# Optimization experiments

Measured on AMD Instinct MI355X. Metric: run time of the kernel, lower is better.

The kernel has to match this reference:

```python
import jax, jax.numpy as jnp
import numpy as np

H, DH = 16, 64            # num heads, head dim
D = H * DH                # hidden size 1024
ALPHA, BW, A, R = 1.0, 1.0, 0.5, 1.0
D_INT = DH                # num_heads > 1 -> d_intrinsic = head_dim
EPS = 1e-12
CLIP = 1.0 - 1e-6         # keep acos (and its grad) finite


def setup_inputs() -> dict:
    key = jax.random.key(0)
    ks = jax.random.split(key, 5)
    w = lambda k: jax.random.normal(k, (D, D), jnp.float32) * 0.02
    return {
        "x": jax.random.normal(ks[0], (4, 1024, D), jnp.float32),
        "wq": w(ks[1]), "bq": jnp.zeros((D,), jnp.float32),
        "wk": w(ks[2]), "bk": jnp.zeros((D,), jnp.float32),
        "wv": w(ks[3]), "bv": jnp.zeros((D,), jnp.float32),
        "wo": w(ks[4]), "bo": jnp.zeros((D,), jnp.float32),
    }


def reference(x, wq, bq, wk, bk, wv, bv, wo, bo):
    B, S, _ = x.shape

    def heads(t):  # [B,S,D] -> [B,H,S,DH]
        return t.reshape(B, S, H, DH).transpose(0, 2, 1, 3)

    def l2norm(t):
        return t / jnp.maximum(jnp.linalg.norm(t, axis=-1, keepdims=True), EPS)

    q = l2norm(heads(x @ wq + bq))
    k = l2norm(heads(x @ wk + bk))
    v = heads(x @ wv + bv)

    # spherical geodesic distance
    dot = jnp.clip(jnp.einsum('bhqd,bhkd->bhqk', q, k), -CLIP, CLIP)
    g_dist = jnp.arccos(dot) * R

    # power-law kernel (alpha < 2 branch)
    attn_score = (1.0 + g_dist / jnp.sqrt(BW)) ** (-(D_INT + ALPHA))

    # bistochastic (Sinkhorn-like) normalization, a > 0 branch
    n_r = attn_score.sum(-1)   # [B,H,S] row sums
    n_c = attn_score.sum(-2)   # [B,H,S] col sums
    k_tilde = (n_r ** (-A))[..., :, None] * attn_score * (n_c ** (-A))[..., None, :]
    probs = k_tilde / jnp.maximum(k_tilde.sum(-1, keepdims=True), EPS)  # L1 row normalize

    out = jnp.einsum('bhqk,bhkd->bhqd', probs, v)
    out = out.transpose(0, 2, 1, 3).reshape(B, S, D)
    return out @ wo + bo
```

## Files before the change

kernel.cpp:

```cpp
#include <hip/hip_runtime.h>
#include <hip/hip_bf16.h>
#include <cstdint>
#include <cstddef>

#define BATCH  4
#define SEQ    1024
#define NHEAD  16
#define DHEAD  64
#define DMODEL 1024
#define NROWS  4096
#define BH     64
#define CLIPV  0.999999f
#define PEXP   65.0f

#define QOFF   133.5f
#define QK_    490.8988764f
#define QINV   0.0020370716f
#define QC     65535.5f

typedef _Float16 h16;
typedef _Float16 half8 __attribute__((ext_vector_type(8)));
typedef _Float16 half4 __attribute__((ext_vector_type(4)));
typedef __fp16   fp16x2 __attribute__((ext_vector_type(2)));
typedef float    f32x4 __attribute__((ext_vector_type(4)));

typedef const __attribute__((address_space(1))) void gas_void;
typedef __attribute__((address_space(3))) void las_void;
#define GLOAD_LDS16(g, l) \
    __builtin_amdgcn_global_load_lds((gas_void*)(g), (las_void*)(l), 16, 0, 0)

__device__ __forceinline__ float spfns_lg(float d) {
    d = __builtin_amdgcn_fmed3f(d, -CLIPV, CLIPV);
    float a = fabsf(d);
    float s = __builtin_amdgcn_sqrtf(1.0f - a);
    float p = -0.0187293f;
    p = fmaf(p, a,  0.0742610f);
    p = fmaf(p, a, -0.2121144f);
    p = fmaf(p, a,  1.5707288f);
    float r = s * p;
    float g = (d >= 0.0f) ? r : (3.14159265358979f - r);
    return __builtin_amdgcn_logf(1.0f + g);
}

__device__ __forceinline__ unsigned pk_h2(float lo, float hi) {
    fp16x2 v = __builtin_amdgcn_cvt_pkrtz(lo, hi);
    return __builtin_bit_cast(unsigned, v);
}

__global__ __launch_bounds__(256) void cvt_x(const float* __restrict__ x,
                                             h16* __restrict__ xh)
{
    size_t i = ((size_t)blockIdx.x * 256 + threadIdx.x) * 8;
    float4 a = *reinterpret_cast<const float4*>(&x[i]);
    float4 b = *reinterpret_cast<const float4*>(&x[i + 4]);
    half8 o;
    o[0]=(h16)a.x; o[1]=(h16)a.y; o[2]=(h16)a.z; o[3]=(h16)a.w;
    o[4]=(h16)b.x; o[5]=(h16)b.y; o[6]=(h16)b.z; o[7]=(h16)b.w;
    *reinterpret_cast<half8*>(&xh[i]) = o;
}

__global__ __launch_bounds__(256) void wtrans(const float* __restrict__ wq,
                                              const float* __restrict__ wk,
                                              const float* __restrict__ wv,
                                              const float* __restrict__ wo,
                                              h16* __restrict__ wt3,
                                              h16* __restrict__ wot)
{
    __shared__ float T[64][65];
    const int k0 = blockIdx.x * 64, d0 = blockIdx.y * 64, z = blockIdx.z;
    const float* src = (z==0)?wq:(z==1)?wk:(z==2)?wv:wo;
    h16* dst = (z==3) ? wot : (wt3 + (size_t)z * 1024 * 1024);
    const int t = threadIdx.x;

    #pragma unroll
    for (int p = 0; p < 4; ++p) {
        int k = (t >> 4) + p * 16;
        int c = (t & 15) * 4;
        float4 v = *reinterpret_cast<const float4*>(&src[(size_t)(k0 + k) * 1024 + d0 + c]);
        T[c + 0][k] = v.x; T[c + 1][k] = v.y; T[c + 2][k] = v.z; T[c + 3][k] = v.w;
    }
    __syncthreads();
    #pragma unroll
    for (int p = 0; p < 2; ++p) {
        int dl = (t >> 3) + p * 32;
        int c  = (t & 7) * 8;
        half8 o;
        #pragma unroll
        for (int e = 0; e < 8; ++e) o[e] = (h16)T[dl][c + e];
        *reinterpret_cast<half8*>(&dst[(size_t)(d0 + dl) * 1024 + k0 + c]) = o;
    }
}

__global__ __launch_bounds__(256) void gemm_f16(const h16* __restrict__ A,
                                                const h16* __restrict__ Bt,
                                                const float* __restrict__ b0,
                                                const float* __restrict__ b1,
                                                const float* __restrict__ b2,
                                                h16* __restrict__ oq,
                                                h16* __restrict__ ok,
                                                h16* __restrict__ ovt,
                                                float* __restrict__ of32,
                                                int mode)
{
    __shared__ __align__(16) h16 As[128][64];
    __shared__ __align__(16) h16 Bs[128][64];
    const int n0 = blockIdx.x * 128, d0 = blockIdx.y * 128;
    const int t = threadIdx.x, l = t & 63, w = t >> 6;
    const int wr = (w >> 1) * 64, wc = (w & 1) * 64;
    const int lr = l >> 3, lc8 = (l & 7) * 8;

    f32x4 acc[4][4];
    #pragma unroll
    for (int i = 0; i < 4; ++i)
        #pragma unroll
        for (int j = 0; j < 4; ++j) acc[i][j] = (f32x4){0.f,0.f,0.f,0.f};

    for (int k0 = 0; k0 < 1024; k0 += 64) {
        __syncthreads();
        #pragma unroll
        for (int q = 0; q < 4; ++q) {
            int r = w * 32 + q * 8;
            GLOAD_LDS16(&A[(size_t)(n0 + r + lr) * 1024 + k0 + lc8], &As[r][0]);
            GLOAD_LDS16(&Bt[(size_t)(d0 + r + lr) * 1024 + k0 + lc8], &Bs[r][0]);
        }
        __syncthreads();
        #pragma unroll
        for (int kk = 0; kk < 2; ++kk) {
            half8 a[4], b[4];
            #pragma unroll
            for (int fi = 0; fi < 4; ++fi)
                a[fi] = *reinterpret_cast<const half8*>(&As[wr + fi*16 + (l & 15)][((l >> 4) * 8) + kk * 32]);
            #pragma unroll
            for (int fj = 0; fj < 4; ++fj)
                b[fj] = *reinterpret_cast<const half8*>(&Bs[wc + fj*16 + (l & 15)][((l >> 4) * 8) + kk * 32]);
            #pragma unroll
            for (int fi = 0; fi < 4; ++fi)
                #pragma unroll
                for (int fj = 0; fj < 4; ++fj)
                    acc[fi][fj] = __builtin_amdgcn_mfma_f32_16x16x32_f16(a[fi], b[fj], acc[fi][fj], 0, 0, 0);
        }
    }

    if (mode == 0) {
        const int dbase = d0 + wc;
        const int mat = dbase >> 10, d1b = dbase & 1023, h = d1b >> 6;
        const float* bp = (mat == 0) ? b0 : (mat == 1) ? b1 : b2;
        #pragma unroll
        for (int fi = 0; fi < 4; ++fi) {
            float vals[4][4];
            #pragma unroll
            for (int fj = 0; fj < 4; ++fj) {
                float bias = bp[d1b + fj * 16 + (l & 15)];
                #pragma unroll
                for (int rr = 0; rr < 4; ++rr) vals[fj][rr] = acc[fi][fj][rr] + bias;
            }
            if (mat < 2) {
                float ss[4];
                #pragma unroll
                for (int rr = 0; rr < 4; ++rr)
                    ss[rr] = vals[0][rr]*vals[0][rr] + vals[1][rr]*vals[1][rr]
                           + vals[2][rr]*vals[2][rr] + vals[3][rr]*vals[3][rr];
                #pragma unroll
                for (int off = 1; off < 16; off <<= 1) {
                    #pragma unroll
                    for (int rr = 0; rr < 4; ++rr) ss[rr] += __shfl_xor(ss[rr], off);
                }
                #pragma unroll
                for (int rr = 0; rr < 4; ++rr) {
                    float sc = __builtin_amdgcn_rcpf(
                        fmaxf(__builtin_amdgcn_sqrtf(ss[rr]), 1e-12f));
                    #pragma unroll
                    for (int fj = 0; fj < 4; ++fj) vals[fj][rr] *= sc;
                }
            }
            const int s0n = n0 + wr + fi * 16 + ((l >> 4) << 2);
            #pragma unroll
            for (int fj = 0; fj < 4; ++fj) {
                int dh = fj * 16 + (l & 15);
                if (mat == 2) {
                    int b = s0n >> 10, s0 = s0n & 1023;
                    half4 o;
                    #pragma unroll
                    for (int rr = 0; rr < 4; ++rr) o[rr] = (h16)vals[fj][rr];
                    *reinterpret_cast<half4*>(&ovt[(((size_t)(b * NHEAD + h)) * DHEAD + dh) * SEQ + s0]) = o;
                } else {
                    h16* dst = (mat == 0) ? oq : ok;
                    #pragma unroll
                    for (int rr = 0; rr < 4; ++rr) {
                        int n = s0n + rr, b = n >> 10, s = n & 1023;
                        dst[(((size_t)(b * NHEAD + h)) * SEQ + s) * DHEAD + dh] = (h16)vals[fj][rr];
                    }
                }
            }
        }
    } else {
        #pragma unroll
        for (int fi = 0; fi < 4; ++fi) {
            #pragma unroll
            for (int fj = 0; fj < 4; ++fj) {
                int d = d0 + wc + fj * 16 + (l & 15);
                int s0n = n0 + wr + fi * 16 + ((l >> 4) << 2);
                float bias = b0[d];
                #pragma unroll
                for (int rr = 0; rr < 4; ++rr) {
                    int n = s0n + rr;
                    of32[(size_t)n * DMODEL + d] = acc[fi][fj][rr] + bias;
                }
            }
        }
    }
}

template<int CACHED>
__global__ __launch_bounds__(256) void passA(const h16* __restrict__ qh,
                                             const h16* __restrict__ kh,
                                             float* __restrict__ nc,
                                             unsigned* __restrict__ rm_u,
                                             int* __restrict__ gacc,
                                             unsigned short* __restrict__ Sw)
{
    __shared__ __align__(16) h16 Ks[32][72];
    __shared__ float red[4][32];
    const int t = threadIdx.x, l = t & 63, w = t >> 6;
    const int id  = blockIdx.y * 32 + blockIdx.x;
    const int nid = (id & 7) * 256 + (id >> 3);
    const int jt = nid & 31, bh = nid >> 5;
    const int j0 = jt * 32;

    {
        int r = t >> 3, c = (t & 7) * 8;
        *reinterpret_cast<half8*>(&Ks[r][c]) =
            *reinterpret_cast<const half8*>(&kh[(((size_t)bh * SEQ) + j0 + r) * DHEAD + c]);
    }
    __syncthreads();

    half8 kfr[2][2];
    #pragma unroll
    for (int f = 0; f < 2; ++f)
        #pragma unroll
        for (int kk = 0; kk < 2; ++kk)
            kfr[f][kk] = *reinterpret_cast<const half8*>(&Ks[f*16 + (l & 15)][((l >> 4) * 8) + kk * 32]);

    float ncacc[8];
    #pragma unroll
    for (int x = 0; x < 8; ++x) ncacc[x] = 0.f;

    const h16* qb = qh + ((size_t)bh * SEQ + w*16 + (l & 15)) * DHEAD + ((l >> 4) * 8);
    half8 nq0 = *reinterpret_cast<const half8*>(qb);
    half8 nq1 = *reinterpret_cast<const half8*>(qb + 32);

    #pragma unroll 2
    for (int it = 0; it < 16; ++it) {
        half8 aq0 = nq0, aq1 = nq1;
        if (it < 15) {
            const h16* qn = qb + (size_t)(it + 1) * 64 * DHEAD;
            nq0 = *reinterpret_cast<const half8*>(qn);
            nq1 = *reinterpret_cast<const half8*>(qn + 32);
        }

        float mloc = 1e30f;
        #pragma unroll
        for (int f = 0; f < 2; ++f) {
            f32x4 cfr = (f32x4){0.f,0.f,0.f,0.f};
            cfr = __builtin_amdgcn_mfma_f32_16x16x32_f16(kfr[f][0], aq0, cfr, 0, 0, 0);
            cfr = __builtin_amdgcn_mfma_f32_16x16x32_f16(kfr[f][1], aq1, cfr, 0, 0, 0);
            unsigned uq[4];
            #pragma unroll
            for (int rr = 0; rr < 4; ++rr) {
                float lg = spfns_lg(cfr[rr]);
                float tt = lg * (-PEXP);
                ncacc[f*4 + rr] += __builtin_amdgcn_exp2f(tt);
                mloc = fminf(mloc, lg);
                if (CACHED) uq[rr] = (unsigned)fmaf(tt, QK_, QC);
            }
            if (CACHED) {
                uint2 pkw;
                pkw.x = uq[0] | (uq[1] << 16);
                pkw.y = uq[2] | (uq[3] << 16);
                size_t sidx = (((((size_t)(bh*16 + (jt >> 1))*16 + it)*4 + w)*4
                               + ((jt & 1)*2 + f)) << 8) + (size_t)l*4;
                *reinterpret_cast<uint2*>(&Sw[sidx]) = pkw;
            }
        }
        mloc = fminf(mloc, __shfl_xor(mloc, 16));
        mloc = fminf(mloc, __shfl_xor(mloc, 32));
        if (l < 16)
            atomicMin(&rm_u[(size_t)bh * SEQ + it*64 + w*16 + l], __float_as_uint(mloc));
    }

    #pragma unroll
    for (int x = 0; x < 8; ++x) {
        #pragma unroll
        for (int off = 1; off < 16; off <<= 1)
            ncacc[x] += __shfl_xor(ncacc[x], off);
    }
    if ((l & 15) == 0) {
        #pragma unroll
        for (int x = 0; x < 8; ++x)
            red[w][(x >> 2) * 16 + (l >> 4) * 4 + (x & 3)] = ncacc[x];
    }
    __syncthreads();
    if (t < 32) {
        float v = red[0][t] + red[1][t] + red[2][t] + red[3][t];
        nc[(size_t)bh * SEQ + j0 + t] = v;
        atomicAdd(gacc, (int)rintf(__builtin_amdgcn_logf(v) * 64.0f));
    }
}

__global__ __launch_bounds__(256) void ncprep(const float* __restrict__ nc,
                                              const unsigned* __restrict__ rm_u,
                                              const int* __restrict__ gacc,
                                              float* __restrict__ lcr,
                                              float* __restrict__ lrm)
{
    int i = blockIdx.x * 256 + threadIdx.x;
    float Lm = (float)(*gacc) / (65536.0f * 64.0f);
    lcr[i] = -0.5f * (__builtin_amdgcn_logf(nc[i]) - Lm);
    lrm[i] = -PEXP * __uint_as_float(rm_u[i]);
}

__global__ __launch_bounds__(256) void passB_c(const h16* __restrict__ vt,
                                               const float* __restrict__ lcr,
                                               const float* __restrict__ lrm,
                                               const unsigned short* __restrict__ Sw,
                                               h16* __restrict__ aoh)
{
    __shared__ __align__(16) h16 Vs[64][72];
    __shared__ __align__(16) h16 Ps[4][16][72];
    const int t = threadIdx.x, l = t & 63, w = t >> 6;
    const int id  = blockIdx.y * 16 + blockIdx.x;
    const int nid = (id & 7) * 128 + (id >> 3);
    const int it = nid & 15, bh = nid >> 4;
    const int i0 = it * 64;

    const float nlr = -lrm[(size_t)bh * SEQ + i0 + w*16 + (l & 15)] - QOFF;

    half8 ones8;
    {
        h16 ov = (h16)(((l & 15) == 0) ? 1.0f : 0.0f);
        #pragma unroll
        for (int e = 0; e < 8; ++e) ones8[e] = ov;
    }

    f32x4 pv[4];
    #pragma unroll
    for (int fd = 0; fd < 4; ++fd) pv[fd] = (f32x4){0.f,0.f,0.f,0.f};
    f32x4 pvden = (f32x4){0.f,0.f,0.f,0.f};

    const int sr = t >> 3, sc = (t & 7) * 8;
    const h16* vsrc = vt + ((size_t)bh * DHEAD + sr) * SEQ + sc;
    const float* lc_base = lcr + (size_t)bh * SEQ + (l >> 4) * 4;

    auto s_ptr = [&](int jc2, int fj) -> const uint2* {
        size_t sidx = (((((size_t)(bh*16 + jc2)*16 + it)*4 + w)*4 + fj) << 8) + (size_t)l*4;
        return reinterpret_cast<const uint2*>(&Sw[sidx]);
    };

    half8 vr0 = *reinterpret_cast<const half8*>(vsrc);
    half8 vr1 = *reinterpret_cast<const half8*>(vsrc + (size_t)32 * SEQ);
    uint2 sv[4];
    float4 lc[4];
    #pragma unroll
    for (int fj = 0; fj < 4; ++fj) {
        sv[fj] = *s_ptr(0, fj);
        lc[fj] = *reinterpret_cast<const float4*>(&lc_base[fj*16]);
    }

    for (int jc = 0; jc < 16; ++jc) {
        __syncthreads();
        *reinterpret_cast<half8*>(&Vs[sr][sc])      = vr0;
        *reinterpret_cast<half8*>(&Vs[sr + 32][sc]) = vr1;
        __syncthreads();

        if (jc < 15) {
            const h16* vn = vsrc + (jc + 1) * 64;
            vr0 = *reinterpret_cast<const half8*>(vn);
            vr1 = *reinterpret_cast<const half8*>(vn + (size_t)32 * SEQ);
        }

        #pragma unroll
        for (int fj = 0; fj < 4; ++fj) {
            float u0 = (float)(sv[fj].x & 0xffffu), u1 = (float)(sv[fj].x >> 16);
            float u2 = (float)(sv[fj].y & 0xffffu), u3 = (float)(sv[fj].y >> 16);
            float pp0 = __builtin_amdgcn_exp2f(fmaf(u0, QINV, lc[fj].x + nlr));
            float pp1 = __builtin_amdgcn_exp2f(fmaf(u1, QINV, lc[fj].y + nlr));
            float pp2 = __builtin_amdgcn_exp2f(fmaf(u2, QINV, lc[fj].z + nlr));
            float pp3 = __builtin_amdgcn_exp2f(fmaf(u3, QINV, lc[fj].w + nlr));
            uint2 pk;
            pk.x = pk_h2(pp0, pp1);
            pk.y = pk_h2(pp2, pp3);
            *reinterpret_cast<uint2*>(&Ps[w][l & 15][fj*16 + (l >> 4) * 4]) = pk;
        }
        if (jc < 15) {
            #pragma unroll
            for (int fj = 0; fj < 4; ++fj) {
                sv[fj] = *s_ptr(jc + 1, fj);
                lc[fj] = *reinterpret_cast<const float4*>(&lc_base[(jc + 1)*64 + fj*16]);
            }
        }

        half8 pa0 = *reinterpret_cast<const half8*>(&Ps[w][l & 15][((l >> 4) * 8)]);
        half8 pa1 = *reinterpret_cast<const half8*>(&Ps[w][l & 15][((l >> 4) * 8) + 32]);
        #pragma unroll
        for (int fd = 0; fd < 4; ++fd) {
            half8 vb0 = *reinterpret_cast<const half8*>(&Vs[fd*16 + (l & 15)][((l >> 4) * 8)]);
            half8 vb1 = *reinterpret_cast<const half8*>(&Vs[fd*16 + (l & 15)][((l >> 4) * 8) + 32]);
            pv[fd] = __builtin_amdgcn_mfma_f32_16x16x32_f16(pa0, vb0, pv[fd], 0, 0, 0);
            pv[fd] = __builtin_amdgcn_mfma_f32_16x16x32_f16(pa1, vb1, pv[fd], 0, 0, 0);
        }
        pvden = __builtin_amdgcn_mfma_f32_16x16x32_f16(pa0, ones8, pvden, 0, 0, 0);
        pvden = __builtin_amdgcn_mfma_f32_16x16x32_f16(pa1, ones8, pvden, 0, 0, 0);
    }

    const int b = bh >> 4, h = bh & 15;
    #pragma unroll
    for (int rr = 0; rr < 4; ++rr) {
        float ds = __shfl(pvden[rr], l & 48);
        float inv = __builtin_amdgcn_rcpf(ds);
        int s = i0 + w * 16 + ((l >> 4) << 2) + rr;
        #pragma unroll
        for (int fd = 0; fd < 4; ++fd) {
            aoh[((size_t)(b * SEQ + s)) * DMODEL + h * DHEAD + fd * 16 + (l & 15)] =
                (h16)(pv[fd][rr] * inv);
        }
    }
}

__global__ __launch_bounds__(256) void passB_r(const h16* __restrict__ qh,
                                               const h16* __restrict__ kh,
                                               const h16* __restrict__ vt,
                                               const float* __restrict__ lcr,
                                               const float* __restrict__ lrm,
                                               h16* __restrict__ aoh)
{
    __shared__ __align__(16) h16 Ks[64][72];
    __shared__ __align__(16) h16 Vs[64][72];
    __shared__ __align__(16) h16 Ps[4][16][72];
    __shared__ float lcr_s[64];
    __shared__ float lrm_s[64];

    const int it = blockIdx.x, bh = blockIdx.y;
    const int i0 = it * 64;
    const int t = threadIdx.x, l = t & 63, w = t >> 6;
    h16* Pflat = &Ps[0][0][0];

    #pragma unroll
    for (int p = 0; p < 2; ++p) {
        int r = (t >> 3) + p * 32, c = (t & 7) * 8;
        *reinterpret_cast<half8*>(&Pflat[r * 72 + c]) =
            *reinterpret_cast<const half8*>(&qh[(((size_t)bh * SEQ) + i0 + r) * DHEAD + c]);
    }
    if (t < 64) lrm_s[t] = lrm[(size_t)bh * SEQ + i0 + t];
    __syncthreads();

    half8 aq0 = *reinterpret_cast<const half8*>(&Pflat[(w*16 + (l & 15)) * 72 + ((l >> 4) * 8)]);
    half8 aq1 = *reinterpret_cast<const half8*>(&Pflat[(w*16 + (l & 15)) * 72 + ((l >> 4) * 8) + 32]);
    const float nlr = -lrm_s[w*16 + (l & 15)];

    half8 ones8;
    {
        h16 ov = (h16)(((l & 15) == 0) ? 1.0f : 0.0f);
        #pragma unroll
        for (int e = 0; e < 8; ++e) ones8[e] = ov;
    }

    f32x4 pv[4];
    #pragma unroll
    for (int fd = 0; fd < 4; ++fd) pv[fd] = (f32x4){0.f,0.f,0.f,0.f};
    f32x4 pvden = (f32x4){0.f,0.f,0.f,0.f};

    for (int jc = 0; jc < 16; ++jc) {
        const int j0 = jc * 64;
        __syncthreads();
        #pragma unroll
        for (int p = 0; p < 2; ++p) {
            int r = (t >> 3) + p * 32, c = (t & 7) * 8;
            *reinterpret_cast<half8*>(&Ks[r][c]) =
                *reinterpret_cast<const half8*>(&kh[(((size_t)bh * SEQ) + j0 + r) * DHEAD + c]);
            *reinterpret_cast<half8*>(&Vs[r][c]) =
                *reinterpret_cast<const half8*>(&vt[(((size_t)bh * DHEAD) + r) * SEQ + j0 + c]);
        }
        if (t < 64) lcr_s[t] = lcr[(size_t)bh * SEQ + j0 + t];
        __syncthreads();

        #pragma unroll
        for (int fj = 0; fj < 4; ++fj) {
            half8 kb0 = *reinterpret_cast<const half8*>(&Ks[fj*16 + (l & 15)][((l >> 4) * 8)]);
            half8 kb1 = *reinterpret_cast<const half8*>(&Ks[fj*16 + (l & 15)][((l >> 4) * 8) + 32]);
            f32x4 cfr = (f32x4){0.f,0.f,0.f,0.f};
            cfr = __builtin_amdgcn_mfma_f32_16x16x32_f16(kb0, aq0, cfr, 0, 0, 0);
            cfr = __builtin_amdgcn_mfma_f32_16x16x32_f16(kb1, aq1, cfr, 0, 0, 0);
            float4 lc4 = *reinterpret_cast<const float4*>(&lcr_s[fj*16 + (l >> 4) * 4]);
            float pp0 = __builtin_amdgcn_exp2f(fmaf(spfns_lg(cfr[0]), -PEXP, lc4.x + nlr));
            float pp1 = __builtin_amdgcn_exp2f(fmaf(spfns_lg(cfr[1]), -PEXP, lc4.y + nlr));
            float pp2 = __builtin_amdgcn_exp2f(fmaf(spfns_lg(cfr[2]), -PEXP, lc4.z + nlr));
            float pp3 = __builtin_amdgcn_exp2f(fmaf(spfns_lg(cfr[3]), -PEXP, lc4.w + nlr));
            uint2 pk;
            pk.x = pk_h2(pp0, pp1);
            pk.y = pk_h2(pp2, pp3);
            *reinterpret_cast<uint2*>(&Ps[w][l & 15][fj*16 + (l >> 4) * 4]) = pk;
        }

        half8 pa0 = *reinterpret_cast<const half8*>(&Ps[w][l & 15][((l >> 4) * 8)]);
        half8 pa1 = *reinterpret_cast<const half8*>(&Ps[w][l & 15][((l >> 4) * 8) + 32]);
        #pragma unroll
        for (int fd = 0; fd < 4; ++fd) {
            half8 vb0 = *reinterpret_cast<const half8*>(&Vs[fd*16 + (l & 15)][((l >> 4) * 8)]);
            half8 vb1 = *reinterpret_cast<const half8*>(&Vs[fd*16 + (l & 15)][((l >> 4) * 8) + 32]);
            pv[fd] = __builtin_amdgcn_mfma_f32_16x16x32_f16(pa0, vb0, pv[fd], 0, 0, 0);
            pv[fd] = __builtin_amdgcn_mfma_f32_16x16x32_f16(pa1, vb1, pv[fd], 0, 0, 0);
        }
        pvden = __builtin_amdgcn_mfma_f32_16x16x32_f16(pa0, ones8, pvden, 0, 0, 0);
        pvden = __builtin_amdgcn_mfma_f32_16x16x32_f16(pa1, ones8, pvden, 0, 0, 0);
    }

    const int b = bh >> 4, h = bh & 15;
    #pragma unroll
    for (int rr = 0; rr < 4; ++rr) {
        float ds = __shfl(pvden[rr], l & 48);
        float inv = __builtin_amdgcn_rcpf(ds);
        int s = i0 + w * 16 + ((l >> 4) << 2) + rr;
        #pragma unroll
        for (int fd = 0; fd < 4; ++fd) {
            aoh[((size_t)(b * SEQ + s)) * DMODEL + h * DHEAD + fd * 16 + (l & 15)] =
                (h16)(pv[fd][rr] * inv);
        }
    }
}

extern "C" void kernel_launch(void* const* d_in, const int* in_sizes, int n_in,
                              void* d_out, int out_size, void* d_ws, size_t ws_size,
                              hipStream_t stream)
{
    (void)in_sizes; (void)n_in; (void)out_size;
    const float* x  = (const float*)d_in[0];
    const float* wq = (const float*)d_in[1];
    const float* bq = (const float*)d_in[2];
    const float* wk = (const float*)d_in[3];
    const float* bk = (const float*)d_in[4];
    const float* wv = (const float*)d_in[5];
    const float* bv = (const float*)d_in[6];
    const float* wo = (const float*)d_in[7];
    const float* bo = (const float*)d_in[8];
    float* out = (float*)d_out;

    h16* ws16 = (h16*)d_ws;
    const size_t NX  = (size_t)NROWS * DMODEL;
    const size_t NW3 = (size_t)3 * DMODEL * DMODEL;
    const size_t NW1 = (size_t)DMODEL * DMODEL;
    const size_t NH  = (size_t)BH * SEQ * DHEAD;
    h16* xh  = ws16;
    h16* wt3 = xh  + NX;
    h16* wot = wt3 + NW3;
    h16* qh  = wot + NW1;
    h16* kh  = qh  + NH;
    h16* vt  = kh  + NH;
    h16* aoh = vt  + NH;
    float* nc  = (float*)(aoh + NX);
    float* lcr = nc  + BH * SEQ;
    float* lrm = lcr + BH * SEQ;
    unsigned* rm_u = (unsigned*)(lrm + BH * SEQ);
    int* gacc = (int*)(rm_u + BH * SEQ);

    size_t used = (size_t)((char*)(gacc + 1) - (char*)d_ws);
    used = (used + 255) & ~(size_t)255;
    unsigned short* Sw = (unsigned short*)((char*)d_ws + used);
    const size_t SBYTES = (size_t)BH * SEQ * SEQ * 2;
    const bool cache = (ws_size >= used + SBYTES);

    hipMemsetAsync(rm_u, 0xFF, (size_t)BH * SEQ * sizeof(unsigned), stream);
    hipMemsetAsync(gacc, 0, sizeof(int), stream);

    cvt_x<<<2048, 256, 0, stream>>>(x, xh);
    wtrans<<<dim3(16, 16, 4), 256, 0, stream>>>(wq, wk, wv, wo, wt3, wot);

    gemm_f16<<<dim3(32, 24), 256, 0, stream>>>(xh, wt3, bq, bk, bv,
                                               qh, kh, vt, nullptr, 0);

    if (cache) {
        passA<1><<<dim3(32, BH), 256, 0, stream>>>(qh, kh, nc, rm_u, gacc, Sw);
        ncprep<<<256, 256, 0, stream>>>(nc, rm_u, gacc, lcr, lrm);
        passB_c<<<dim3(16, BH), 256, 0, stream>>>(vt, lcr, lrm, Sw, aoh);
    } else {
        passA<0><<<dim3(32, BH), 256, 0, stream>>>(qh, kh, nc, rm_u, gacc, Sw);
        ncprep<<<256, 256, 0, stream>>>(nc, rm_u, gacc, lcr, lrm);
        passB_r<<<dim3(16, BH), 256, 0, stream>>>(qh, kh, vt, lcr, lrm, aoh);
    }

    gemm_f16<<<dim3(32, 8), 256, 0, stream>>>(aoh, wot, bo, nullptr, nullptr,
                                              nullptr, nullptr, nullptr, out, 1);
}
```

Before: 180.9 us.

## Fold column scaling into V and denominator vector; use nontemporal score-cache accesses

```diff
diff --git a/kernel.cpp b/kernel.cpp
--- a/kernel.cpp
+++ b/kernel.cpp
@@ -23,6 +23,7 @@
 typedef _Float16 half4 __attribute__((ext_vector_type(4)));
 typedef __fp16   fp16x2 __attribute__((ext_vector_type(2)));
 typedef float    f32x4 __attribute__((ext_vector_type(4)));
+typedef unsigned uint2v __attribute__((ext_vector_type(2)));
 
 typedef const __attribute__((address_space(1))) void gas_void;
 typedef __attribute__((address_space(3))) void las_void;
@@ -45,6 +46,13 @@
 __device__ __forceinline__ unsigned pk_h2(float lo, float hi) {
     fp16x2 v = __builtin_amdgcn_cvt_pkrtz(lo, hi);
     return __builtin_bit_cast(unsigned, v);
+}
+
+__device__ __forceinline__ half8 h8_zero() {
+    half8 z;
+    #pragma unroll
+    for (int e = 0; e < 8; ++e) z[e] = (h16)0.f;
+    return z;
 }
 
 __global__ __launch_bounds__(256) void cvt_x(const float* __restrict__ x,
@@ -245,6 +253,14 @@
     #pragma unroll
     for (int x = 0; x < 8; ++x) ncacc[x] = 0.f;
 
+    unsigned short* sp[2] = {nullptr, nullptr};
+    if (CACHED) {
+        size_t base = ((((size_t)(bh*16 + (jt >> 1))*16)*16 + w*4 + (jt & 1)*2) << 8)
+                      + (size_t)l*4;
+        sp[0] = Sw + base;
+        sp[1] = sp[0] + 256;
+    }
+
     const h16* qb = qh + ((size_t)bh * SEQ + w*16 + (l & 15)) * DHEAD + ((l >> 4) * 8);
     half8 nq0 = *reinterpret_cast<const half8*>(qb);
     half8 nq1 = *reinterpret_cast<const half8*>(qb + 32);
@@ -274,14 +290,13 @@
                 if (CACHED) uq[rr] = (unsigned)fmaf(tt, QK_, QC);
             }
             if (CACHED) {
-                uint2 pkw;
-                pkw.x = uq[0] | (uq[1] << 16);
-                pkw.y = uq[2] | (uq[3] << 16);
-                size_t sidx = (((((size_t)(bh*16 + (jt >> 1))*16 + it)*4 + w)*4
-                               + ((jt & 1)*2 + f)) << 8) + (size_t)l*4;
-                *reinterpret_cast<uint2*>(&Sw[sidx]) = pkw;
+                uint2v pkw;
+                pkw[0] = uq[0] | (uq[1] << 16);
+                pkw[1] = uq[2] | (uq[3] << 16);
+                __builtin_nontemporal_store(pkw, reinterpret_cast<uint2v*>(sp[f]));
             }
         }
+        if (CACHED) { sp[0] += 4096; sp[1] += 4096; }
         mloc = fminf(mloc, __shfl_xor(mloc, 16));
         mloc = fminf(mloc, __shfl_xor(mloc, 32));
         if (l < 16)
@@ -319,8 +334,32 @@
     lrm[i] = -PEXP * __uint_as_float(rm_u[i]);
 }
 
+__global__ __launch_bounds__(256) void vscale(h16* __restrict__ vt,
+                                              const float* __restrict__ lcr,
+                                              h16* __restrict__ fh)
+{
+    size_t gid = (size_t)blockIdx.x * 256 + threadIdx.x;
+    int jb  = (int)(gid & 127) * 8;
+    int bh  = (int)(gid >> 13);
+    int dhq = (int)(gid >> 7) & 63;
+    const float* lp = lcr + (size_t)bh * SEQ + jb;
+    float f[8];
+    #pragma unroll
+    for (int e = 0; e < 8; ++e) f[e] = __builtin_amdgcn_exp2f(lp[e]);
+    half8 v = *reinterpret_cast<half8*>(&vt[gid * 8]);
+    #pragma unroll
+    for (int e = 0; e < 8; ++e) v[e] = (h16)((float)v[e] * f[e]);
+    *reinterpret_cast<half8*>(&vt[gid * 8]) = v;
+    if (dhq == 0) {
+        half8 ff;
+        #pragma unroll
+        for (int e = 0; e < 8; ++e) ff[e] = (h16)f[e];
+        *reinterpret_cast<half8*>(&fh[(size_t)bh * SEQ + jb]) = ff;
+    }
+}
+
 __global__ __launch_bounds__(256) void passB_c(const h16* __restrict__ vt,
-                                               const float* __restrict__ lcr,
+                                               const h16* __restrict__ fh,
                                                const float* __restrict__ lrm,
                                                const unsigned short* __restrict__ Sw,
                                                h16* __restrict__ aoh)
@@ -334,13 +373,7 @@
     const int i0 = it * 64;
 
     const float nlr = -lrm[(size_t)bh * SEQ + i0 + w*16 + (l & 15)] - QOFF;
-
-    half8 ones8;
-    {
-        h16 ov = (h16)(((l & 15) == 0) ? 1.0f : 0.0f);
-        #pragma unroll
-        for (int e = 0; e < 8; ++e) ones8[e] = ov;
-    }
+    const bool den_lane = (l & 15) == 0;
 
     f32x4 pv[4];
     #pragma unroll
@@ -349,21 +382,22 @@
 
     const int sr = t >> 3, sc = (t & 7) * 8;
     const h16* vsrc = vt + ((size_t)bh * DHEAD + sr) * SEQ + sc;
-    const float* lc_base = lcr + (size_t)bh * SEQ + (l >> 4) * 4;
-
-    auto s_ptr = [&](int jc2, int fj) -> const uint2* {
+    const h16* fsrc = fh + (size_t)bh * SEQ + (l >> 4) * 8;
+
+    auto s_ptr = [&](int jc2, int fj) -> const uint2v* {
         size_t sidx = (((((size_t)(bh*16 + jc2)*16 + it)*4 + w)*4 + fj) << 8) + (size_t)l*4;
-        return reinterpret_cast<const uint2*>(&Sw[sidx]);
+        return reinterpret_cast<const uint2v*>(&Sw[sidx]);
     };
 
     half8 vr0 = *reinterpret_cast<const half8*>(vsrc);
     half8 vr1 = *reinterpret_cast<const half8*>(vsrc + (size_t)32 * SEQ);
-    uint2 sv[4];
-    float4 lc[4];
-    #pragma unroll
-    for (int fj = 0; fj < 4; ++fj) {
-        sv[fj] = *s_ptr(0, fj);
-        lc[fj] = *reinterpret_cast<const float4*>(&lc_base[fj*16]);
+    uint2v sv[4];
+    #pragma unroll
+    for (int fj = 0; fj < 4; ++fj) sv[fj] = __builtin_nontemporal_load(s_ptr(0, fj));
+    half8 fa = h8_zero(), fb = h8_zero();
+    if (den_lane) {
+        fa = *reinterpret_cast<const half8*>(fsrc);
+        fb = *reinterpret_cast<const half8*>(fsrc + 32);
     }
 
     for (int jc = 0; jc < 16; ++jc) {
@@ -380,22 +414,26 @@
 
         #pragma unroll
         for (int fj = 0; fj < 4; ++fj) {
-            float u0 = (float)(sv[fj].x & 0xffffu), u1 = (float)(sv[fj].x >> 16);
-            float u2 = (float)(sv[fj].y & 0xffffu), u3 = (float)(sv[fj].y >> 16);
-            float pp0 = __builtin_amdgcn_exp2f(fmaf(u0, QINV, lc[fj].x + nlr));
-            float pp1 = __builtin_amdgcn_exp2f(fmaf(u1, QINV, lc[fj].y + nlr));
-            float pp2 = __builtin_amdgcn_exp2f(fmaf(u2, QINV, lc[fj].z + nlr));
-            float pp3 = __builtin_amdgcn_exp2f(fmaf(u3, QINV, lc[fj].w + nlr));
-            uint2 pk;
-            pk.x = pk_h2(pp0, pp1);
-            pk.y = pk_h2(pp2, pp3);
-            *reinterpret_cast<uint2*>(&Ps[w][l & 15][fj*16 + (l >> 4) * 4]) = pk;
-        }
+            float u0 = (float)(sv[fj][0] & 0xffffu), u1 = (float)(sv[fj][0] >> 16);
+            float u2 = (float)(sv[fj][1] & 0xffffu), u3 = (float)(sv[fj][1] >> 16);
+            float pp0 = __builtin_amdgcn_exp2f(fmaf(u0, QINV, nlr));
+            float pp1 = __builtin_amdgcn_exp2f(fmaf(u1, QINV, nlr));
+            float pp2 = __builtin_amdgcn_exp2f(fmaf(u2, QINV, nlr));
+            float pp3 = __builtin_amdgcn_exp2f(fmaf(u3, QINV, nlr));
+            uint2v pk;
+            pk[0] = pk_h2(pp0, pp1);
+            pk[1] = pk_h2(pp2, pp3);
+            *reinterpret_cast<uint2v*>(&Ps[w][l & 15][fj*16 + (l >> 4) * 4]) = pk;
+        }
+
+        half8 cfa = fa, cfb = fb;
         if (jc < 15) {
             #pragma unroll
-            for (int fj = 0; fj < 4; ++fj) {
-                sv[fj] = *s_ptr(jc + 1, fj);
-                lc[fj] = *reinterpret_cast<const float4*>(&lc_base[(jc + 1)*64 + fj*16]);
+            for (int fj = 0; fj < 4; ++fj)
+                sv[fj] = __builtin_nontemporal_load(s_ptr(jc + 1, fj));
+            if (den_lane) {
+                fa = *reinterpret_cast<const half8*>(fsrc + (jc + 1) * 64);
+                fb = *reinterpret_cast<const half8*>(fsrc + (jc + 1) * 64 + 32);
             }
         }
 
@@ -408,8 +446,8 @@
             pv[fd] = __builtin_amdgcn_mfma_f32_16x16x32_f16(pa0, vb0, pv[fd], 0, 0, 0);
             pv[fd] = __builtin_amdgcn_mfma_f32_16x16x32_f16(pa1, vb1, pv[fd], 0, 0, 0);
         }
-        pvden = __builtin_amdgcn_mfma_f32_16x16x32_f16(pa0, ones8, pvden, 0, 0, 0);
-        pvden = __builtin_amdgcn_mfma_f32_16x16x32_f16(pa1, ones8, pvden, 0, 0, 0);
+        pvden = __builtin_amdgcn_mfma_f32_16x16x32_f16(pa0, cfa, pvden, 0, 0, 0);
+        pvden = __builtin_amdgcn_mfma_f32_16x16x32_f16(pa1, cfb, pvden, 0, 0, 0);
     }
 
     const int b = bh >> 4, h = bh & 15;
@@ -457,11 +495,10 @@
     half8 aq1 = *reinterpret_cast<const half8*>(&Pflat[(w*16 + (l & 15)) * 72 + ((l >> 4) * 8) + 32]);
     const float nlr = -lrm_s[w*16 + (l & 15)];
 
-    half8 ones8;
-    {
-        h16 ov = (h16)(((l & 15) == 0) ? 1.0f : 0.0f);
-        #pragma unroll
-        for (int e = 0; e < 8; ++e) ones8[e] = ov;
+    half8 ones8 = h8_zero();
+    if ((l & 15) == 0) {
+        #pragma unroll
+        for (int e = 0; e < 8; ++e) ones8[e] = (h16)1.0f;
     }
 
     f32x4 pv[4];
@@ -495,10 +532,10 @@
             float pp1 = __builtin_amdgcn_exp2f(fmaf(spfns_lg(cfr[1]), -PEXP, lc4.y + nlr));
             float pp2 = __builtin_amdgcn_exp2f(fmaf(spfns_lg(cfr[2]), -PEXP, lc4.z + nlr));
             float pp3 = __builtin_amdgcn_exp2f(fmaf(spfns_lg(cfr[3]), -PEXP, lc4.w + nlr));
-            uint2 pk;
-            pk.x = pk_h2(pp0, pp1);
-            pk.y = pk_h2(pp2, pp3);
-            *reinterpret_cast<uint2*>(&Ps[w][l & 15][fj*16 + (l >> 4) * 4]) = pk;
+            uint2v pk;
+            pk[0] = pk_h2(pp0, pp1);
+            pk[1] = pk_h2(pp2, pp3);
+            *reinterpret_cast<uint2v*>(&Ps[w][l & 15][fj*16 + (l >> 4) * 4]) = pk;
         }
 
         half8 pa0 = *reinterpret_cast<const half8*>(&Ps[w][l & 15][((l >> 4) * 8)]);
@@ -561,8 +598,9 @@
     float* lrm = lcr + BH * SEQ;
     unsigned* rm_u = (unsigned*)(lrm + BH * SEQ);
     int* gacc = (int*)(rm_u + BH * SEQ);
-
-    size_t used = (size_t)((char*)(gacc + 1) - (char*)d_ws);
+    h16* fh = (h16*)(gacc + 1);
+
+    size_t used = (size_t)((char*)(fh + BH * SEQ) - (char*)d_ws);
     used = (used + 255) & ~(size_t)255;
     unsigned short* Sw = (unsigned short*)((char*)d_ws + used);
     const size_t SBYTES = (size_t)BH * SEQ * SEQ * 2;
@@ -580,7 +618,8 @@
     if (cache) {
         passA<1><<<dim3(32, BH), 256, 0, stream>>>(qh, kh, nc, rm_u, gacc, Sw);
         ncprep<<<256, 256, 0, stream>>>(nc, rm_u, gacc, lcr, lrm);
-        passB_c<<<dim3(16, BH), 256, 0, stream>>>(vt, lcr, lrm, Sw, aoh);
+        vscale<<<2048, 256, 0, stream>>>(vt, lcr, fh);
+        passB_c<<<dim3(16, BH), 256, 0, stream>>>(vt, fh, lrm, Sw, aoh);
     } else {
         passA<0><<<dim3(32, BH), 256, 0, stream>>>(qh, kh, nc, rm_u, gacc, Sw);
         ncprep<<<256, 256, 0, stream>>>(nc, rm_u, gacc, lcr, lrm);
```

Result: slower. 192.8 us (+6.6%).
